# Kernel optimization log

Measured on AMD Instinct MI355X. Metric: run time of the kernel, lower is better.

## Reference

```python
import jax, jax.numpy as jnp
import numpy as np

IN_FEATURES = 4096
OUT_FEATURES = 4096
N_TOKENS = 1024

@jax.custom_vjp
def binarize(w):
    # UnipolarSte.forward: (w > 0).float()
    return (w > 0).astype(w.dtype)

def _bin_fwd(w):
    return binarize(w), None

def _bin_bwd(_, g):
    # UnipolarSte.backward: F.hardtanh(grad_output) == clip(g, -1, 1)
    return (jnp.clip(g, -1.0, 1.0),)

binarize.defvjp(_bin_fwd, _bin_bwd)

def setup_inputs() -> dict:
    key = jax.random.key(0)
    kx, kw = jax.random.split(key)
    x = jax.random.normal(kx, (N_TOKENS, IN_FEATURES), dtype=jnp.float32)
    weight = jax.random.normal(kw, (OUT_FEATURES, IN_FEATURES), dtype=jnp.float32)
    scaling_factor = jnp.ones((OUT_FEATURES,), dtype=jnp.float32)
    return {"x": x, "weight": weight, "scaling_factor": scaling_factor}

def reference(x, weight, scaling_factor):
    w_b = binarize(weight)                      # [out, in] in {0,1}
    out = jnp.einsum('ni,oi->no', x, w_b)       # F.linear(x, w_b)
    # s_eff = round(clamp(s,1)).detach() - s.detach() + s
    s_round = jax.lax.stop_gradient(jnp.round(jnp.clip(scaling_factor, 1.0, None)))
    s_eff = s_round - jax.lax.stop_gradient(scaling_factor) + scaling_factor
    return out * s_eff[None, :]
```

## Files before the change

kernel.cpp:

```cpp
#include <hip/hip_runtime.h>

#define M_TOK 1024
#define NOUT  4096
#define KIN   4096

typedef __attribute__((ext_vector_type(8))) short bf16x8_t;
typedef __attribute__((ext_vector_type(4))) float f32x4_t;


__device__ __forceinline__ unsigned pack_bf16(float a, float b) {
  unsigned ua = __float_as_uint(a);
  unsigned ub = __float_as_uint(b);
  ua = (ua + 0x7FFFu + ((ua >> 16) & 1u)) >> 16;
  ub = (ub + 0x7FFFu + ((ub >> 16) & 1u)) >> 16;
  return ua | (ub << 16);
}

__device__ __forceinline__ unsigned bits8(float4 a, float4 b) {
  return  (unsigned)(a.x > 0.f)        | ((unsigned)(a.y > 0.f) << 1) |
         ((unsigned)(a.z > 0.f) << 2)  | ((unsigned)(a.w > 0.f) << 3) |
         ((unsigned)(b.x > 0.f) << 4)  | ((unsigned)(b.y > 0.f) << 5) |
         ((unsigned)(b.z > 0.f) << 6)  | ((unsigned)(b.w > 0.f) << 7);
}

__global__ __launch_bounds__(256) void prep_wx(const float4* __restrict__ w4,
                                               unsigned short* __restrict__ bfrag,
                                               const float4* __restrict__ x4,
                                               uint4* __restrict__ xfrag) {
  const unsigned bb = blockIdx.x;
  if (bb < 4096) {
    const unsigned t = bb * 256 + threadIdx.x;
    const int l16 = t & 15, quad = (t >> 4) & 3;
    const int kt = (t >> 6) & 63, n16 = t >> 12;
    const int n = n16 * 16 + l16;
    const float4* p = w4 + (size_t)n * (KIN / 4) + kt * 16 + quad * 2;
    float4 f0 = p[0], f1 = p[1];
    float4 f2 = p[8], f3 = p[9];
    const unsigned b0 = bits8(f0, f1);
    const unsigned b1 = bits8(f2, f3);
    bfrag[t] = (unsigned short)(b0 | (b1 << 8));
  } else {
    const unsigned t = (bb - 4096) * 256 + threadIdx.x;
    const int l = t & 63;
    const unsigned f = t >> 6;
    const int m16 = f >> 7, k32 = f & 127;
    const int row = m16 * 16 + (l & 15);
    const int c4  = k32 * 8 + (l >> 4) * 2;
    const float4* p = x4 + (size_t)row * (KIN / 4) + c4;
    float4 a = p[0], b = p[1];
    uint4 o;
    o.x = pack_bf16(a.x, a.y);
    o.y = pack_bf16(a.z, a.w);
    o.z = pack_bf16(b.x, b.y);
    o.w = pack_bf16(b.z, b.w);
    xfrag[t] = o;
  }
}

__global__ __launch_bounds__(256, 2) void gemm_bin_kernel(
    const unsigned short* __restrict__ Xf,
    const unsigned short* __restrict__ Bf,
    const float* __restrict__ sf,
    float* __restrict__ C) {
  const int tid  = threadIdx.x;
  const int lane = tid & 63;
  const int wave = tid >> 6;
  const int quad = lane >> 4;
  const int l16  = lane & 15;
  const unsigned bid = blockIdx.x;
  const int xcd = bid & 7, idx = bid >> 3;
  const int m0 = (xcd * 2 + (idx >> 5)) * 64;
  const int n0 = (idx & 31) * 128;
  const int wn = wave * 32;
  const int m16b = m0 >> 4;
  const int n16b = (n0 + wn) >> 4;

  const uint4* Xf4 = (const uint4*)Xf;

  f32x4_t acc[4][2];
#pragma unroll
  for (int i = 0; i < 4; ++i)
#pragma unroll
    for (int j = 0; j < 2; ++j)
      acc[i][j] = (f32x4_t){0.f, 0.f, 0.f, 0.f};

  uint4 a[2][4][2];
  unsigned b[2][2];

  auto LOAD = [&](int u, int kt) {
#pragma unroll
    for (int i = 0; i < 4; ++i)
#pragma unroll
      for (int ks = 0; ks < 2; ++ks)
        a[u][i][ks] = Xf4[((size_t)(m16b + i) * 128 + kt * 2 + ks) * 64 + lane];
#pragma unroll
    for (int j = 0; j < 2; ++j)
      b[u][j] = (unsigned)Bf[((n16b + j) * 64 + kt) * 64 + lane];
  };

  auto COMP = [&](int u) {
#pragma unroll
    for (int j = 0; j < 2; ++j)
#pragma unroll
      for (int ks = 0; ks < 2; ++ks) {
        unsigned byte = (b[u][j] >> (ks * 8)) & 0xFFu;
        union { unsigned u32[4]; bf16x8_t v; } ex;
#pragma unroll
        for (int p = 0; p < 4; ++p) {
          unsigned tt = (byte >> (2 * p)) & 3u;
          ex.u32[p] = ((tt | (tt << 15)) & 0x10001u) * 0x3F80u;
        }
#pragma unroll
        for (int i = 0; i < 4; ++i) {
          union { uint4 q; bf16x8_t v; } av;
          av.q = a[u][i][ks];
          acc[i][j] = __builtin_amdgcn_mfma_f32_16x16x32_bf16(av.v, ex.v, acc[i][j], 0, 0, 0);
        }
      }
  };

  LOAD(0, 0);
  for (int kt = 0; kt < 64; kt += 2) {
    LOAD(1, kt + 1);
    COMP(0);
    if (kt + 2 < 64) LOAD(0, kt + 2);
    COMP(1);
  }

#pragma unroll
  for (int j = 0; j < 2; ++j) {
    const int n = n0 + wn + j * 16 + l16;
    const float s = rintf(fmaxf(sf[n], 1.0f));
#pragma unroll
    for (int i = 0; i < 4; ++i) {
      const int mr = m0 + i * 16 + quad * 4;
#pragma unroll
      for (int r = 0; r < 4; ++r)
        C[(size_t)(mr + r) * NOUT + n] = acc[i][j][r] * s;
    }
  }
}

extern "C" void kernel_launch(void* const* d_in, const int* in_sizes, int n_in,
                              void* d_out, int out_size, void* d_ws, size_t ws_size,
                              hipStream_t stream) {
  const float* x  = (const float*)d_in[0];
  const float* w  = (const float*)d_in[1];
  const float* sf = (const float*)d_in[2];
  float* out = (float*)d_out;

  unsigned short* Bfrag = (unsigned short*)d_ws;
  unsigned short* Xfrag = (unsigned short*)((char*)d_ws + (4u << 20));

  prep_wx<<<6144, 256, 0, stream>>>((const float4*)w, Bfrag, (const float4*)x,
                                    (uint4*)Xfrag);
  gemm_bin_kernel<<<512, 256, 0, stream>>>(Xfrag, Bfrag, sf, out);
}
```

Measured before the change: 145.4 us.

## Stage X fragments through LDS and retile waves to a 2x2 grid

The GEMM kernel now loads the X (activation) fragments into a double-buffered LDS tile with global_load_lds, so each X fragment comes from global memory once per block. Previously each of the four waves loaded all 64 rows itself. Waves are rearranged into a 2x2 grid of 32x64 sub-tiles, so each wave reads half as many X fragments and twice as many B fragments. The binary weight expansion is cheaper: a shift-and-mask makes bf16 2.0 instead of 1.0, and a 0.5 factor in the epilogue compensates. The cost is two __syncthreads per K pair and extra LDS traffic.

Result: slower. 154.5 us (+6.3%).

```diff
diff --git a/kernel.cpp b/kernel.cpp
--- a/kernel.cpp
+++ b/kernel.cpp
@@ -21,6 +21,12 @@
          ((unsigned)(a.z > 0.f) << 2)  | ((unsigned)(a.w > 0.f) << 3) |
          ((unsigned)(b.x > 0.f) << 4)  | ((unsigned)(b.y > 0.f) << 5) |
          ((unsigned)(b.z > 0.f) << 6)  | ((unsigned)(b.w > 0.f) << 7);
+}
+
+__device__ __forceinline__ void gload_lds16(const uint4* g, uint4* l) {
+  __builtin_amdgcn_global_load_lds(
+      (const __attribute__((address_space(1))) unsigned*)g,
+      (__attribute__((address_space(3))) unsigned*)l, 16, 0, 0);
 }
 
 __global__ __launch_bounds__(256) void prep_wx(const float4* __restrict__ w4,
@@ -62,78 +68,101 @@
     const unsigned short* __restrict__ Bf,
     const float* __restrict__ sf,
     float* __restrict__ C) {
+  __shared__ uint4 lds[2][4][4][64];
   const int tid  = threadIdx.x;
   const int lane = tid & 63;
   const int wave = tid >> 6;
+  const int wm   = wave >> 1;
+  const int wq   = wave & 1;
   const int quad = lane >> 4;
   const int l16  = lane & 15;
   const unsigned bid = blockIdx.x;
   const int xcd = bid & 7, idx = bid >> 3;
   const int m0 = (xcd * 2 + (idx >> 5)) * 64;
   const int n0 = (idx & 31) * 128;
-  const int wn = wave * 32;
   const int m16b = m0 >> 4;
-  const int n16b = (n0 + wn) >> 4;
+  const int n16b = (n0 >> 4) + wq * 4;
 
   const uint4* Xf4 = (const uint4*)Xf;
 
-  f32x4_t acc[4][2];
+  f32x4_t acc[2][4];
 #pragma unroll
-  for (int i = 0; i < 4; ++i)
+  for (int i = 0; i < 2; ++i)
 #pragma unroll
-    for (int j = 0; j < 2; ++j)
+    for (int j = 0; j < 4; ++j)
       acc[i][j] = (f32x4_t){0.f, 0.f, 0.f, 0.f};
 
-  uint4 a[2][4][2];
-  unsigned b[2][2];
-
-  auto LOAD = [&](int u, int kt) {
+  auto STAGE = [&](uint4 (&L)[4][4][64], int it) {
+    const uint4* src = Xf4 + ((size_t)(m16b + wave) * 128 + it * 4) * 64 + lane;
 #pragma unroll
-    for (int i = 0; i < 4; ++i)
-#pragma unroll
-      for (int ks = 0; ks < 2; ++ks)
-        a[u][i][ks] = Xf4[((size_t)(m16b + i) * 128 + kt * 2 + ks) * 64 + lane];
-#pragma unroll
-    for (int j = 0; j < 2; ++j)
-      b[u][j] = (unsigned)Bf[((n16b + j) * 64 + kt) * 64 + lane];
+    for (int q = 0; q < 4; ++q)
+      gload_lds16(src + q * 64, &L[wave][q][0]);
   };
 
-  auto COMP = [&](int u) {
+  auto LOADB = [&](unsigned (&bb)[2][4], int it) {
 #pragma unroll
-    for (int j = 0; j < 2; ++j)
+    for (int s = 0; s < 2; ++s)
 #pragma unroll
-      for (int ks = 0; ks < 2; ++ks) {
-        unsigned byte = (b[u][j] >> (ks * 8)) & 0xFFu;
-        union { unsigned u32[4]; bf16x8_t v; } ex;
+      for (int j = 0; j < 4; ++j)
+        bb[s][j] = (unsigned)Bf[((n16b + j) * 64 + it * 2 + s) * 64 + lane];
+  };
+
+  auto READA = [&](uint4 (&af)[2][4], const uint4 (&L)[4][4][64]) {
 #pragma unroll
-        for (int p = 0; p < 4; ++p) {
-          unsigned tt = (byte >> (2 * p)) & 3u;
-          ex.u32[p] = ((tt | (tt << 15)) & 0x10001u) * 0x3F80u;
-        }
+    for (int i = 0; i < 2; ++i)
 #pragma unroll
-        for (int i = 0; i < 4; ++i) {
-          union { uint4 q; bf16x8_t v; } av;
-          av.q = a[u][i][ks];
-          acc[i][j] = __builtin_amdgcn_mfma_f32_16x16x32_bf16(av.v, ex.v, acc[i][j], 0, 0, 0);
+      for (int h = 0; h < 4; ++h)
+        af[i][h] = L[wm * 2 + i][h][lane];
+  };
+
+  auto COMP = [&](const uint4 (&af)[2][4], const unsigned (&bb)[2][4]) {
+#pragma unroll
+    for (int s = 0; s < 2; ++s)
+#pragma unroll
+      for (int j = 0; j < 4; ++j) {
+        const unsigned br = bb[s][j];
+#pragma unroll
+        for (int ks = 0; ks < 2; ++ks) {
+          union { unsigned u32[4]; bf16x8_t v; } ex;
+#pragma unroll
+          for (int p = 0; p < 4; ++p)
+            ex.u32[p] = ((br << (14 - 8 * ks - 2 * p)) |
+                         (br << (29 - 8 * ks - 2 * p))) & 0x40004000u;
+#pragma unroll
+          for (int i = 0; i < 2; ++i) {
+            union { uint4 q; bf16x8_t v; } av;
+            av.q = af[i][s * 2 + ks];
+            acc[i][j] = __builtin_amdgcn_mfma_f32_16x16x32_bf16(av.v, ex.v, acc[i][j], 0, 0, 0);
+          }
         }
       }
   };
 
-  LOAD(0, 0);
-  for (int kt = 0; kt < 64; kt += 2) {
-    LOAD(1, kt + 1);
-    COMP(0);
-    if (kt + 2 < 64) LOAD(0, kt + 2);
-    COMP(1);
+  unsigned bA[2][4], bB[2][4];
+  uint4 af[2][4];
+
+  STAGE(lds[0], 0);
+  LOADB(bA, 0);
+  __syncthreads();
+
+  for (int it = 0; it < 32; it += 2) {
+    if (it + 1 < 32) { STAGE(lds[1], it + 1); LOADB(bB, it + 1); }
+    READA(af, lds[0]);
+    COMP(af, bA);
+    __syncthreads();
+    if (it + 2 < 32) { STAGE(lds[0], it + 2); LOADB(bA, it + 2); }
+    READA(af, lds[1]);
+    COMP(af, bB);
+    __syncthreads();
   }
 
 #pragma unroll
-  for (int j = 0; j < 2; ++j) {
-    const int n = n0 + wn + j * 16 + l16;
-    const float s = rintf(fmaxf(sf[n], 1.0f));
+  for (int j = 0; j < 4; ++j) {
+    const int n = n0 + wq * 64 + j * 16 + l16;
+    const float s = rintf(fmaxf(sf[n], 1.0f)) * 0.5f;
 #pragma unroll
-    for (int i = 0; i < 4; ++i) {
-      const int mr = m0 + i * 16 + quad * 4;
+    for (int i = 0; i < 2; ++i) {
+      const int mr = m0 + wm * 32 + i * 16 + quad * 4;
 #pragma unroll
       for (int r = 0; r < 4; ++r)
         C[(size_t)(mr + r) * NOUT + n] = acc[i][j][r] * s;
```
